# Kernel tuning notes

Measured on AMD Instinct MI355X. Metric: run time of the kernel, lower is better.

## Reference

```python
import jax, jax.numpy as jnp
import numpy as np

BASE_R = 0.1      # base_radius (compared against squared distances)
K = 20            # PositionEncoder k
H = 0.1           # dilated_ball_query bandwidth
EPS_BN = 1e-5


def _gelu(x):
    return jax.nn.gelu(x, approximate=False)  # torch nn.GELU default (erf)


def _bn(x, g, b):
    # eval-mode BatchNorm (running_mean=0, running_var=1), channel axis = 1
    shape = (1, -1) + (1,) * (x.ndim - 2)
    scale = g / np.float32(np.sqrt(1.0 + EPS_BN))
    return x * scale.reshape(shape) + b.reshape(shape)


def _conv1x1(x, w):
    # pointwise conv (no bias): w [out_c, in_c], x [B, in_c, ...]
    return jnp.einsum('oc,bc...->bo...', w, x)


def _l1norm(x, axis):
    # F.normalize(p=1): divide by L1 norm clamped to 1e-12
    return x / jnp.maximum(jnp.sum(jnp.abs(x), axis=axis, keepdims=True), 1e-12)


def _forward(xyz, w_q, g_q, b_q, w_k, g_k, b_k, w_v, g_v, b_v,
             w_pe, b_pe, g_pe, bb_pe, w_m1, g_m1, b_m1, w_m2, g_m2, b_m2,
             w_out, g_out, b_out):
    B, _, N = xyz.shape
    # ---- pairwise squared distances [B,N,N] ----
    sq = jnp.sum(xyz * xyz, axis=1)
    dist = -2.0 * jnp.einsum('bcn,bcm->bnm', xyz, xyz) + sq[:, :, None] + sq[:, None, :]
    # ---- dilated ball query (sigma=1) ----
    gauss = jnp.exp(-dist / (2.0 * H * H))
    kd = jnp.sum(gauss, axis=-1, keepdims=True)                 # [B,N,1]
    kd_score = kd / (jnp.max(kd, axis=1, keepdims=True) + 1e-9)
    radius = BASE_R + BASE_R * kd_score                         # max_radius = 2*base
    keep = dist < radius                                        # [B,N,N]
    # ---- masked attention (emb_cent == emb_x == cat(xyz, xyz)) ----
    emb = jnp.concatenate([xyz, xyz], axis=1)                   # [B,6,N]
    q = _bn(_conv1x1(emb, w_q), g_q, b_q)                       # [B,1,N]
    k_ = _bn(_conv1x1(emb, w_k), g_k, b_k)                      # [B,1,N]
    scores = jnp.einsum('bhn,bhm->bnm', q, k_)                  # [B,N,N]
    scores = jnp.where(keep, scores, -1e9)
    adj = jax.nn.softmax(scores, axis=-1)
    adj = _l1norm(_l1norm(adj, 1), -1)                          # doubly L1-normalized
    # ---- graph smoothing + value conv ----
    smoothed = jnp.einsum('bcn,bnm->bcm', xyz, adj)
    variation = smoothed - xyz
    v = _bn(_conv1x1(jnp.concatenate([variation, xyz], axis=1), w_v), g_v, b_v)  # [B,64,N]
    # ---- position encoder: ball-query top-k neighbor gather ----
    ar = jnp.arange(N, dtype=jnp.int32)[None, None, :]
    idx = jnp.where(dist > radius, N, ar)                       # mark out-of-ball with N
    idx = jnp.sort(idx, axis=-1)[:, :, :K]                      # k nearest-index in-ball
    idx = jnp.where(idx == N, idx[:, :, :1], idx)               # pad with first neighbor
    grouped = jax.vmap(lambda f, i: f[:, i])(xyz, idx)          # [B,3,N,K]
    pts = jnp.broadcast_to(xyz[:, :, :, None], grouped.shape)
    pf = jnp.concatenate([pts, grouped, grouped - pts], axis=1)  # [B,9,N,K]
    pf = _conv1x1(pf, w_pe) + b_pe[None, :, None, None]          # conv2d 1x1 with bias
    pf = _gelu(_bn(pf, g_pe, bb_pe))
    pf = jnp.max(pf, axis=-1)                                    # [B,out/8,N]
    pf = _gelu(_bn(_conv1x1(pf, w_m1), g_m1, b_m1))              # [B,out/4,N]
    pos = _bn(_conv1x1(pf, w_m2), g_m2, b_m2)                    # [B,out,N]
    out = _gelu(v + pos)
    return _bn(_conv1x1(out, w_out), g_out, b_out)               # [B,32,N]


def setup_inputs() -> dict:
    key = jax.random.key(0)
    ks = iter(jax.random.split(key, 40))
    B, N, OC = 4, 4096, 64

    def w(shape):
        return jax.random.normal(next(ks), shape, jnp.float32) / np.float32(np.sqrt(shape[-1]))

    def gb(c):
        g = 1.0 + 0.1 * jax.random.normal(next(ks), (c,), jnp.float32)
        b = 0.1 * jax.random.normal(next(ks), (c,), jnp.float32)
        return g, b

    xyz = jax.random.uniform(next(ks), (B, 3, N), jnp.float32)
    g_q, b_q = gb(1)
    g_k, b_k = gb(1)
    g_v, b_v = gb(OC)
    g_pe, bb_pe = gb(OC // 8)
    g_m1, b_m1 = gb(OC // 4)
    g_m2, b_m2 = gb(OC)
    g_out, b_out = gb(32)
    return {
        'xyz': xyz,
        'w_q': w((1, 6)), 'g_q': g_q, 'b_q': b_q,
        'w_k': w((1, 6)), 'g_k': g_k, 'b_k': b_k,
        'w_v': w((OC, 6)), 'g_v': g_v, 'b_v': b_v,
        'w_pe': w((OC // 8, 9)), 'b_pe': 0.1 * jax.random.normal(next(ks), (OC // 8,), jnp.float32),
        'g_pe': g_pe, 'bb_pe': bb_pe,
        'w_m1': w((OC // 4, OC // 8)), 'g_m1': g_m1, 'b_m1': b_m1,
        'w_m2': w((OC, OC // 4)), 'g_m2': g_m2, 'b_m2': b_m2,
        'w_out': w((32, OC)), 'g_out': g_out, 'b_out': b_out,
    }


def reference(xyz, w_q, g_q, b_q, w_k, g_k, b_k, w_v, g_v, b_v,
              w_pe, b_pe, g_pe, bb_pe, w_m1, g_m1, b_m1, w_m2, g_m2, b_m2,
              w_out, g_out, b_out):
    return _forward(xyz, w_q, g_q, b_q, w_k, g_k, b_k, w_v, g_v, b_v,
                    w_pe, b_pe, g_pe, bb_pe, w_m1, g_m1, b_m1, w_m2, g_m2, b_m2,
                    w_out, g_out, b_out)
```

## Files before the change

### kernel.cpp

```cpp
#include <hip/hip_runtime.h>
#include <math.h>

#define BB 4
#define NN 4096
#define KNBR 20
#define BN (BB * NN)
#define NSLICE 8
#define SLEN (NN / NSLICE)
#define JPW (SLEN / 16)

__device__ __forceinline__ float gelu_f(float x) {
    return 0.5f * x * (1.0f + erff(x * 0.70710678118654752440f));
}

__global__ void k0_prep(const float* __restrict__ xyz,
                        const float* __restrict__ w_q, const float* __restrict__ g_q, const float* __restrict__ b_q,
                        const float* __restrict__ w_k, const float* __restrict__ g_k, const float* __restrict__ b_k,
                        float* __restrict__ qv, float* __restrict__ kv, float4* __restrict__ pts4) {
    int t = blockIdx.x * blockDim.x + threadIdx.x;
    if (t >= BN) return;
    int b = t / NN, n = t % NN;
    const float* base = xyz + (size_t)b * 3 * NN;
    float x = base[n], y = base[NN + n], z = base[2 * NN + n];
    float sq = x * x + y * y + z * z;
    const float invs = rsqrtf(1.0f + 1e-5f);
    float qr = x * (w_q[0] + w_q[3]) + y * (w_q[1] + w_q[4]) + z * (w_q[2] + w_q[5]);
    float kr = x * (w_k[0] + w_k[3]) + y * (w_k[1] + w_k[4]) + z * (w_k[2] + w_k[5]);
    qv[t] = qr * (g_q[0] * invs) + b_q[0];
    kv[t] = kr * (g_k[0] * invs) + b_k[0];
    pts4[t] = make_float4(x, y, z, sq);
}


__global__ __launch_bounds__(1024, 8)
void p1_kd(const float4* __restrict__ pts4, float* __restrict__ part) {
    __shared__ float s_red[16][256];
    int tid = threadIdx.x;
    int wave = __builtin_amdgcn_readfirstlane(tid >> 6);
    int lane = tid & 63;
    int g = blockIdx.x >> 3, slice = blockIdx.x & 7;
    int b = g >> 4;
    const float4* rb = pts4 + (size_t)b * NN + slice * SLEN + wave * JPW;
    float4 fr[4];
    float acc[4] = {0.f, 0.f, 0.f, 0.f};
    #pragma unroll
    for (int rr = 0; rr < 4; ++rr) fr[rr] = pts4[g * 256 + rr * 64 + lane];
    #pragma unroll 4
    for (int j = 0; j < JPW; ++j) {
        float4 fc = rb[j];
        #pragma unroll
        for (int rr = 0; rr < 4; ++rr) {
            float dot = fr[rr].x * fc.x + fr[rr].y * fc.y + fr[rr].z * fc.z;
            float d = fmaf(-2.0f, dot, fr[rr].w) + fc.w;
            acc[rr] += __expf(-50.0f * d);
        }
    }
    #pragma unroll
    for (int rr = 0; rr < 4; ++rr) s_red[wave][rr * 64 + lane] = acc[rr];
    __syncthreads();
    if (tid < 256) {
        float s = 0.f;
        #pragma unroll
        for (int w = 0; w < 16; ++w) s += s_red[w][tid];
        part[slice * BN + g * 256 + tid] = s;
    }
}

__global__ void k2_radius(const float* __restrict__ part, const float4* __restrict__ pts4,
                          const float* __restrict__ qv, const float* __restrict__ kv,
                          float* __restrict__ radius, float4* __restrict__ recB) {
    int b = blockIdx.x;
    int t = threadIdx.x;
    float kdv[4];
    float mx = -1e30f;
    #pragma unroll
    for (int j = 0; j < 4; ++j) {
        int n = b * NN + j * 1024 + t;
        float s = 0.f;
        #pragma unroll
        for (int c = 0; c < NSLICE; ++c) s += part[c * BN + n];
        kdv[j] = s;
        mx = fmaxf(mx, s);
    }
    __shared__ float red[1024];
    red[t] = mx;
    __syncthreads();
    for (int s = 512; s > 0; s >>= 1) {
        if (t < s) red[t] = fmaxf(red[t], red[t + s]);
        __syncthreads();
    }
    float kmax = red[0];
    #pragma unroll
    for (int j = 0; j < 4; ++j) {
        int n = b * NN + j * 1024 + t;
        float rad = 0.1f + 0.1f * (kdv[j] / (kmax + 1e-9f));
        radius[n] = rad;
        recB[2 * n] = pts4[n];
        recB[2 * n + 1] = make_float4(kv[n], qv[n], rad, 0.f);
    }
}

__global__ __launch_bounds__(1024, 8)
void p3_Zk7(const float4* __restrict__ recB, const float4* __restrict__ pts4,
            const float* __restrict__ radius, float* __restrict__ part,
            int* __restrict__ idxg) {
    __shared__ float s_red[16][256];
    int tid = threadIdx.x;
    int wave = __builtin_amdgcn_readfirstlane(tid >> 6);
    int lane = tid & 63;
    int g = blockIdx.x >> 3, slice = blockIdx.x & 7;
    int b = g >> 4;
    const float4* rb = recB + ((size_t)b * NN + slice * SLEN + wave * JPW) * 2;
    float4 fr[4];
    float q[4], rad[4];
    float acc[4] = {0.f, 0.f, 0.f, 0.f};
    #pragma unroll
    for (int rr = 0; rr < 4; ++rr) {
        int r = g * 256 + rr * 64 + lane;
        fr[rr] = recB[2 * r];
        float4 a = recB[2 * r + 1];
        q[rr] = a.y;
        rad[rr] = a.z;
    }
    #pragma unroll 4
    for (int j = 0; j < JPW; ++j) {
        float4 fc = rb[2 * j];
        float4 an = rb[2 * j + 1];
        #pragma unroll
        for (int rr = 0; rr < 4; ++rr) {
            float dot = fr[rr].x * fc.x + fr[rr].y * fc.y + fr[rr].z * fc.z;
            float d = fmaf(-2.0f, dot, fr[rr].w) + fc.w;
            float e = __expf(q[rr] * an.x);
            acc[rr] += (d < rad[rr]) ? e : 0.f;
        }
    }
    #pragma unroll
    for (int rr = 0; rr < 4; ++rr) s_red[wave][rr * 64 + lane] = acc[rr];
    __syncthreads();
    if (tid < 256) {
        float s = 0.f;
        #pragma unroll
        for (int w = 0; w < 16; ++w) s += s_red[w][tid];
        part[slice * BN + g * 256 + tid] = s;
    }
    int gw = blockIdx.x * 16 + wave;
    for (int rr = 0; rr < 2; ++rr) {
        int row7 = gw * 2 + rr;
        int b7 = row7 / NN;
        const float4* p7 = pts4 + (size_t)b7 * NN;
        float4 f7 = pts4[row7];
        float rad7 = radius[row7];
        int total = 0, firstm = 0;
        bool have = false;
        unsigned long long lmask = (1ULL << lane) - 1ULL;
        for (int i = 0; i < NN / 64 && total < KNBR; ++i) {
            int m = i * 64 + lane;
            float4 fc = p7[m];
            float dot = f7.x * fc.x + f7.y * fc.y + f7.z * fc.z;
            float d = fmaf(-2.0f, dot, f7.w) + fc.w;
            bool inb = !(d > rad7);
            unsigned long long mask = __ballot(inb);
            if (!have && mask != 0ULL) {
                int src7 = __ffsll(mask) - 1;
                firstm = __shfl(m, src7);
                have = true;
            }
            int pos = total + (int)__popcll(mask & lmask);
            if (inb && pos < KNBR) idxg[(size_t)row7 * KNBR + pos] = m;
            total += (int)__popcll(mask);
        }
        if (total < KNBR && lane >= total && lane < KNBR)
            idxg[(size_t)row7 * KNBR + lane] = firstm;
    }
}

__global__ void r3_Z(const float* __restrict__ part, const float4* __restrict__ pts4,
                     const float* __restrict__ qv, const float* __restrict__ radius,
                     float* __restrict__ Z, float4* __restrict__ recC) {
    int t = blockIdx.x * blockDim.x + threadIdx.x;
    float s = 0.f;
    #pragma unroll
    for (int c = 0; c < NSLICE; ++c) s += part[c * BN + t];
    Z[t] = s;
    recC[2 * t] = pts4[t];
    recC[2 * t + 1] = make_float4(qv[t], radius[t], __logf(s), 0.f);
}

__global__ __launch_bounds__(1024, 8)
void p4_colsum(const float4* __restrict__ recC, const float4* __restrict__ recB,
               float* __restrict__ part) {
    __shared__ float s_red[16][256];
    int tid = threadIdx.x;
    int wave = __builtin_amdgcn_readfirstlane(tid >> 6);
    int lane = tid & 63;
    int g = blockIdx.x >> 3, slice = blockIdx.x & 7;
    int b = g >> 4;
    const float4* rb = recC + ((size_t)b * NN + slice * SLEN + wave * JPW) * 2;
    float4 fcc[4];
    float km[4];
    float acc[4] = {0.f, 0.f, 0.f, 0.f};
    #pragma unroll
    for (int rr = 0; rr < 4; ++rr) {
        int c = g * 256 + rr * 64 + lane;
        fcc[rr] = recB[2 * c];
        km[rr] = recB[2 * c + 1].x;
    }
    #pragma unroll 4
    for (int j = 0; j < JPW; ++j) {
        float4 fc = rb[2 * j];
        float4 an = rb[2 * j + 1];
        #pragma unroll
        for (int rr = 0; rr < 4; ++rr) {
            float dot = fc.x * fcc[rr].x + fc.y * fcc[rr].y + fc.z * fcc[rr].z;
            float d = fmaf(-2.0f, dot, fc.w) + fcc[rr].w;
            float e = __expf(an.x * km[rr] - an.z);
            acc[rr] += (d < an.y) ? e : 0.f;
        }
    }
    #pragma unroll
    for (int rr = 0; rr < 4; ++rr) s_red[wave][rr * 64 + lane] = acc[rr];
    __syncthreads();
    if (tid < 256) {
        float s = 0.f;
        #pragma unroll
        for (int w = 0; w < 16; ++w) s += s_red[w][tid];
        part[slice * BN + g * 256 + tid] = s;
    }
}

__global__ void r4_colsum(const float* __restrict__ part, const float4* __restrict__ pts4,
                          const float* __restrict__ kv, float* __restrict__ colsum,
                          float4* __restrict__ recD) {
    int t = blockIdx.x * blockDim.x + threadIdx.x;
    float s = 0.f;
    #pragma unroll
    for (int c = 0; c < NSLICE; ++c) s += part[c * BN + t];
    s = fmaxf(s, 1e-12f);
    colsum[t] = s;
    recD[2 * t] = pts4[t];
    recD[2 * t + 1] = make_float4(kv[t], __logf(s), 0.f, 0.f);
}

__global__ __launch_bounds__(1024, 8)
void p5_rs(const float4* __restrict__ recD, const float4* __restrict__ recB,
           float* __restrict__ part) {
    __shared__ float s_red[16][256];
    int tid = threadIdx.x;
    int wave = __builtin_amdgcn_readfirstlane(tid >> 6);
    int lane = tid & 63;
    int g = blockIdx.x >> 3, slice = blockIdx.x & 7;
    int b = g >> 4;
    const float4* rb = recD + ((size_t)b * NN + slice * SLEN + wave * JPW) * 2;
    float4 fr[4];
    float q[4], rad[4];
    float acc[4] = {0.f, 0.f, 0.f, 0.f};
    #pragma unroll
    for (int rr = 0; rr < 4; ++rr) {
        int r = g * 256 + rr * 64 + lane;
        fr[rr] = recB[2 * r];
        float4 a = recB[2 * r + 1];
        q[rr] = a.y;
        rad[rr] = a.z;
    }
    #pragma unroll 4
    for (int j = 0; j < JPW; ++j) {
        float4 fc = rb[2 * j];
        float4 an = rb[2 * j + 1];
        #pragma unroll
        for (int rr = 0; rr < 4; ++rr) {
            float dot = fr[rr].x * fc.x + fr[rr].y * fc.y + fr[rr].z * fc.z;
            float d = fmaf(-2.0f, dot, fr[rr].w) + fc.w;
            float e = __expf(q[rr] * an.x - an.y);
            acc[rr] += (d < rad[rr]) ? e : 0.f;
        }
    }
    #pragma unroll
    for (int rr = 0; rr < 4; ++rr) s_red[wave][rr * 64 + lane] = acc[rr];
    __syncthreads();
    if (tid < 256) {
        float s = 0.f;
        #pragma unroll
        for (int w = 0; w < 16; ++w) s += s_red[w][tid];
        part[slice * BN + g * 256 + tid] = s;
    }
}

__global__ void r5_rs(const float* __restrict__ part, const float* __restrict__ Z,
                      const float4* __restrict__ recC, const float4* __restrict__ pts4,
                      float4* __restrict__ recE) {
    int t = blockIdx.x * blockDim.x + threadIdx.x;
    float s = 0.f;
    #pragma unroll
    for (int c = 0; c < NSLICE; ++c) s += part[c * BN + t];
    float rs = fmaxf(s / Z[t], 1e-12f);
    float4 a = recC[2 * t + 1];
    recE[2 * t] = pts4[t];
    recE[2 * t + 1] = make_float4(a.x, a.y, a.z + __logf(rs), 0.f);
}

__global__ __launch_bounds__(1024, 8)
void p6_smooth(const float4* __restrict__ recE, const float4* __restrict__ recB,
               float* __restrict__ partx, float* __restrict__ party,
               float* __restrict__ partz) {
    __shared__ float s_rx[16][256];
    __shared__ float s_ry[16][256];
    __shared__ float s_rz[16][256];
    int tid = threadIdx.x;
    int wave = __builtin_amdgcn_readfirstlane(tid >> 6);
    int lane = tid & 63;
    int g = blockIdx.x >> 3, slice = blockIdx.x & 7;
    int b = g >> 4;
    const float4* rb = recE + ((size_t)b * NN + slice * SLEN + wave * JPW) * 2;
    float4 fcc[4];
    float km[4];
    float ax[4] = {0.f, 0.f, 0.f, 0.f};
    float ay[4] = {0.f, 0.f, 0.f, 0.f};
    float az[4] = {0.f, 0.f, 0.f, 0.f};
    #pragma unroll
    for (int rr = 0; rr < 4; ++rr) {
        int c = g * 256 + rr * 64 + lane;
        fcc[rr] = recB[2 * c];
        km[rr] = recB[2 * c + 1].x;
    }
    #pragma unroll 2
    for (int j = 0; j < JPW; ++j) {
        float4 fc = rb[2 * j];
        float4 an = rb[2 * j + 1];
        #pragma unroll
        for (int rr = 0; rr < 4; ++rr) {
            float dot = fc.x * fcc[rr].x + fc.y * fcc[rr].y + fc.z * fcc[rr].z;
            float d = fmaf(-2.0f, dot, fc.w) + fcc[rr].w;
            float w = __expf(an.x * km[rr] - an.z);
            w = (d < an.y) ? w : 0.f;
            ax[rr] += fc.x * w;
            ay[rr] += fc.y * w;
            az[rr] += fc.z * w;
        }
    }
    #pragma unroll
    for (int rr = 0; rr < 4; ++rr) {
        s_rx[wave][rr * 64 + lane] = ax[rr];
        s_ry[wave][rr * 64 + lane] = ay[rr];
        s_rz[wave][rr * 64 + lane] = az[rr];
    }
    __syncthreads();
    if (tid < 256) {
        float sx = 0.f, sy = 0.f, sz = 0.f;
        #pragma unroll
        for (int w = 0; w < 16; ++w) {
            sx += s_rx[w][tid];
            sy += s_ry[w][tid];
            sz += s_rz[w][tid];
        }
        int o = slice * BN + g * 256 + tid;
        partx[o] = sx;
        party[o] = sy;
        partz[o] = sz;
    }
}

__global__ void k8_final(const float* __restrict__ xyz,
                         const float* __restrict__ partx, const float* __restrict__ party,
                         const float* __restrict__ partz, const float* __restrict__ colsum,
                         const int* __restrict__ idxg,
                         const float* __restrict__ w_v, const float* __restrict__ g_v, const float* __restrict__ b_v,
                         const float* __restrict__ w_pe, const float* __restrict__ b_pe,
                         const float* __restrict__ g_pe, const float* __restrict__ bb_pe,
                         const float* __restrict__ w_m1, const float* __restrict__ g_m1, const float* __restrict__ b_m1,
                         const float* __restrict__ w_m2, const float* __restrict__ g_m2, const float* __restrict__ b_m2,
                         const float* __restrict__ w_out, const float* __restrict__ g_out, const float* __restrict__ b_out,
                         float* __restrict__ out) {
    __shared__ float s_pf8[32][9];
    __shared__ float s_pf16[32][17];
    __shared__ float s_g64[32][65];
    int tid = threadIdx.x;
    int ptL = tid >> 3, o = tid & 7;
    int p = blockIdx.x * 32 + ptL;
    int b = p / NN, n = p % NN;
    const float* xb = xyz + (size_t)b * 3 * NN;
    float x = xb[n], y = xb[NN + n], z = xb[2 * NN + n];
    const float invs = rsqrtf(1.0f + 1e-5f);

    float w0 = w_pe[o * 9 + 0], w1 = w_pe[o * 9 + 1], w2 = w_pe[o * 9 + 2];
    float w3 = w_pe[o * 9 + 3], w4 = w_pe[o * 9 + 4], w5 = w_pe[o * 9 + 5];
    float w6 = w_pe[o * 9 + 6], w7 = w_pe[o * 9 + 7], w8 = w_pe[o * 9 + 8];
    float bp = b_pe[o], gp = g_pe[o] * invs, bbp = bb_pe[o];
    float mx = -1e30f;
    for (int kk = 0; kk < KNBR; ++kk) {
        int j = idxg[(size_t)p * KNBR + kk];
        float gx = xb[j], gy = xb[NN + j], gz = xb[2 * NN + j];
        float dx = gx - x, dy = gy - y, dz = gz - z;
        float s = w0 * x + w1 * y + w2 * z + w3 * gx + w4 * gy + w5 * gz
                + w6 * dx + w7 * dy + w8 * dz + bp;
        s = gelu_f(s * gp + bbp);
        mx = fmaxf(mx, s);
    }
    s_pf8[ptL][o] = mx;
    __syncthreads();

    #pragma unroll
    for (int rr = 0; rr < 2; ++rr) {
        int r = o + rr * 8;
        const float* w = w_m1 + r * 8;
        float s = 0.f;
        #pragma unroll
        for (int c = 0; c < 8; ++c) s += w[c] * s_pf8[ptL][c];
        s_pf16[ptL][r] = gelu_f(s * (g_m1[r] * invs) + b_m1[r]);
    }
    __syncthreads();

    float inv = 1.0f / colsum[p];
    float sx = 0.f, sy = 0.f, sz = 0.f;
    #pragma unroll
    for (int c = 0; c < NSLICE; ++c) {
        sx += partx[c * BN + p];
        sy += party[c * BN + p];
        sz += partz[c * BN + p];
    }
    float vx = sx * inv - x, vy = sy * inv - y, vz = sz * inv - z;
    #pragma unroll
    for (int i = 0; i < 8; ++i) {
        int ch = o * 8 + i;
        const float* wm = w_m2 + ch * 16;
        float pos = 0.f;
        #pragma unroll
        for (int c = 0; c < 16; ++c) pos += wm[c] * s_pf16[ptL][c];
        pos = pos * (g_m2[ch] * invs) + b_m2[ch];
        const float* wv = w_v + ch * 6;
        float vv = wv[0] * vx + wv[1] * vy + wv[2] * vz + wv[3] * x + wv[4] * y + wv[5] * z;
        vv = vv * (g_v[ch] * invs) + b_v[ch];
        s_g64[ptL][ch] = gelu_f(vv + pos);
    }
    __syncthreads();

    #pragma unroll
    for (int i = 0; i < 4; ++i) {
        int ch = o * 4 + i;
        const float* w = w_out + ch * 64;
        float s = 0.f;
        #pragma unroll
        for (int c = 0; c < 64; ++c) s += w[c] * s_g64[ptL][c];
        out[((size_t)b * 32 + ch) * NN + n] = s * (g_out[ch] * invs) + b_out[ch];
    }
}

extern "C" void kernel_launch(void* const* d_in, const int* in_sizes, int n_in,
                              void* d_out, int out_size, void* d_ws, size_t ws_size,
                              hipStream_t stream) {
    const float* xyz  = (const float*)d_in[0];
    const float* w_q  = (const float*)d_in[1];
    const float* g_q  = (const float*)d_in[2];
    const float* b_q  = (const float*)d_in[3];
    const float* w_k  = (const float*)d_in[4];
    const float* g_k  = (const float*)d_in[5];
    const float* b_k  = (const float*)d_in[6];
    const float* w_v  = (const float*)d_in[7];
    const float* g_v  = (const float*)d_in[8];
    const float* b_v  = (const float*)d_in[9];
    const float* w_pe = (const float*)d_in[10];
    const float* b_pe = (const float*)d_in[11];
    const float* g_pe = (const float*)d_in[12];
    const float* bb_pe= (const float*)d_in[13];
    const float* w_m1 = (const float*)d_in[14];
    const float* g_m1 = (const float*)d_in[15];
    const float* b_m1 = (const float*)d_in[16];
    const float* w_m2 = (const float*)d_in[17];
    const float* g_m2 = (const float*)d_in[18];
    const float* b_m2 = (const float*)d_in[19];
    const float* w_out= (const float*)d_in[20];
    const float* g_out= (const float*)d_in[21];
    const float* b_out= (const float*)d_in[22];

    float* ws = (float*)d_ws;
    float*  qv     = ws;
    float*  kv     = ws + (size_t)1  * BN;
    float4* pts4   = (float4*)(ws + (size_t)2  * BN);
    float*  radius = ws + (size_t)6  * BN;
    float*  Zv     = ws + (size_t)7  * BN;
    float*  colsum = ws + (size_t)8  * BN;
    float4* recB   = (float4*)(ws + (size_t)9  * BN);
    float4* recC   = (float4*)(ws + (size_t)17 * BN);
    float4* recD   = (float4*)(ws + (size_t)25 * BN);
    float4* recE   = (float4*)(ws + (size_t)33 * BN);
    int*    idxg   = (int*)   (ws + (size_t)41 * BN);
    float*  part1  = ws + (size_t)61 * BN;
    float*  part3  = ws + (size_t)69 * BN;
    float*  part5  = ws + (size_t)77 * BN;
    float*  part7  = ws + (size_t)85 * BN;
    float*  partx  = ws + (size_t)93 * BN;
    float*  party  = ws + (size_t)101 * BN;
    float*  partz  = ws + (size_t)109 * BN;

    const int PB = (BN / 256) * NSLICE;

    k0_prep<<<BN / 256, 256, 0, stream>>>(xyz, w_q, g_q, b_q, w_k, g_k, b_k, qv, kv, pts4);
    p1_kd<<<PB, 1024, 0, stream>>>(pts4, part1);
    k2_radius<<<BB, 1024, 0, stream>>>(part1, pts4, qv, kv, radius, recB);
    p3_Zk7<<<PB, 1024, 0, stream>>>(recB, pts4, radius, part3, idxg);
    r3_Z<<<BN / 256, 256, 0, stream>>>(part3, pts4, qv, radius, Zv, recC);
    p4_colsum<<<PB, 1024, 0, stream>>>(recC, recB, part5);
    r4_colsum<<<BN / 256, 256, 0, stream>>>(part5, pts4, kv, colsum, recD);
    p5_rs<<<PB, 1024, 0, stream>>>(recD, recB, part7);
    r5_rs<<<BN / 256, 256, 0, stream>>>(part7, Zv, recC, pts4, recE);
    p6_smooth<<<PB, 1024, 0, stream>>>(recE, recB, partx, party, partz);
    k8_final<<<BN / 32, 256, 0, stream>>>(xyz, partx, party, partz, colsum, idxg,
                                          w_v, g_v, b_v,
                                          w_pe, b_pe, g_pe, bb_pe,
                                          w_m1, g_m1, b_m1,
                                          w_m2, g_m2, b_m2,
                                          w_out, g_out, b_out,
                                          (float*)d_out);
}
```

Before: 251.6 us.

## Fold prep and reduction kernels into pass kernels, reuse single record buffer

Removes k0_prep and the three small reduction kernels (r3_Z, r4_colsum, r5_rs). Each pass kernel now sums the previous pass's slice partials for its own column slice into shared memory, and p1 builds point records directly from xyz. The separate per-pass record buffers go away, so every pass reads the one recB buffer. This cuts four kernel launches and several global round trips, at the cost of redundant partial-sum and log work repeated across row-group blocks and strided record reads inside p1.

```diff
diff --git a/kernel.cpp b/kernel.cpp
--- a/kernel.cpp
+++ b/kernel.cpp
@@ -13,41 +13,31 @@
     return 0.5f * x * (1.0f + erff(x * 0.70710678118654752440f));
 }
 
-__global__ void k0_prep(const float* __restrict__ xyz,
-                        const float* __restrict__ w_q, const float* __restrict__ g_q, const float* __restrict__ b_q,
-                        const float* __restrict__ w_k, const float* __restrict__ g_k, const float* __restrict__ b_k,
-                        float* __restrict__ qv, float* __restrict__ kv, float4* __restrict__ pts4) {
-    int t = blockIdx.x * blockDim.x + threadIdx.x;
-    if (t >= BN) return;
-    int b = t / NN, n = t % NN;
-    const float* base = xyz + (size_t)b * 3 * NN;
-    float x = base[n], y = base[NN + n], z = base[2 * NN + n];
-    float sq = x * x + y * y + z * z;
-    const float invs = rsqrtf(1.0f + 1e-5f);
-    float qr = x * (w_q[0] + w_q[3]) + y * (w_q[1] + w_q[4]) + z * (w_q[2] + w_q[5]);
-    float kr = x * (w_k[0] + w_k[3]) + y * (w_k[1] + w_k[4]) + z * (w_k[2] + w_k[5]);
-    qv[t] = qr * (g_q[0] * invs) + b_q[0];
-    kv[t] = kr * (g_k[0] * invs) + b_k[0];
-    pts4[t] = make_float4(x, y, z, sq);
+__device__ __forceinline__ float4 mkrec(const float* __restrict__ xb, int n) {
+    float x = xb[n], y = xb[NN + n], z = xb[2 * NN + n];
+    float sq = fmaf(x, x, fmaf(y, y, z * z));
+    return make_float4(x, y, z, sq);
 }
 
 
 __global__ __launch_bounds__(1024, 8)
-void p1_kd(const float4* __restrict__ pts4, float* __restrict__ part) {
+void p1_kd(const float* __restrict__ xyz, float* __restrict__ part) {
     __shared__ float s_red[16][256];
     int tid = threadIdx.x;
     int wave = __builtin_amdgcn_readfirstlane(tid >> 6);
     int lane = tid & 63;
     int g = blockIdx.x >> 3, slice = blockIdx.x & 7;
     int b = g >> 4;
-    const float4* rb = pts4 + (size_t)b * NN + slice * SLEN + wave * JPW;
+    const float* xb = xyz + (size_t)b * 3 * NN;
+    int nbase = (g & 15) * 256;
     float4 fr[4];
     float acc[4] = {0.f, 0.f, 0.f, 0.f};
     #pragma unroll
-    for (int rr = 0; rr < 4; ++rr) fr[rr] = pts4[g * 256 + rr * 64 + lane];
+    for (int rr = 0; rr < 4; ++rr) fr[rr] = mkrec(xb, nbase + rr * 64 + lane);
+    int m0 = slice * SLEN + wave * JPW;
     #pragma unroll 4
     for (int j = 0; j < JPW; ++j) {
-        float4 fc = rb[j];
+        float4 fc = mkrec(xb, m0 + j);
         #pragma unroll
         for (int rr = 0; rr < 4; ++rr) {
             float dot = fr[rr].x * fc.x + fr[rr].y * fc.y + fr[rr].z * fc.z;
@@ -66,11 +56,14 @@
     }
 }
 
-__global__ void k2_radius(const float* __restrict__ part, const float4* __restrict__ pts4,
-                          const float* __restrict__ qv, const float* __restrict__ kv,
-                          float* __restrict__ radius, float4* __restrict__ recB) {
+__global__ void k2_radius(const float* __restrict__ part, const float* __restrict__ xyz,
+                          const float* __restrict__ w_q, const float* __restrict__ g_q, const float* __restrict__ b_q,
+                          const float* __restrict__ w_k, const float* __restrict__ g_k, const float* __restrict__ b_k,
+                          float4* __restrict__ recB) {
     int b = blockIdx.x;
     int t = threadIdx.x;
+    const float* xb = xyz + (size_t)b * 3 * NN;
+    const float invs = rsqrtf(1.0f + 1e-5f);
     float kdv[4];
     float mx = -1e30f;
     #pragma unroll
@@ -92,17 +85,21 @@
     float kmax = red[0];
     #pragma unroll
     for (int j = 0; j < 4; ++j) {
-        int n = b * NN + j * 1024 + t;
+        int nl = j * 1024 + t;
+        int n = b * NN + nl;
         float rad = 0.1f + 0.1f * (kdv[j] / (kmax + 1e-9f));
-        radius[n] = rad;
-        recB[2 * n] = pts4[n];
-        recB[2 * n + 1] = make_float4(kv[n], qv[n], rad, 0.f);
+        float4 r = mkrec(xb, nl);
+        float qr = r.x * (w_q[0] + w_q[3]) + r.y * (w_q[1] + w_q[4]) + r.z * (w_q[2] + w_q[5]);
+        float kr = r.x * (w_k[0] + w_k[3]) + r.y * (w_k[1] + w_k[4]) + r.z * (w_k[2] + w_k[5]);
+        float q = qr * (g_q[0] * invs) + b_q[0];
+        float k = kr * (g_k[0] * invs) + b_k[0];
+        recB[2 * n] = r;
+        recB[2 * n + 1] = make_float4(k, q, rad, 0.f);
     }
 }
 
 __global__ __launch_bounds__(1024, 8)
-void p3_Zk7(const float4* __restrict__ recB, const float4* __restrict__ pts4,
-            const float* __restrict__ radius, float* __restrict__ part,
+void p3_Zk7(const float4* __restrict__ recB, float* __restrict__ part,
             int* __restrict__ idxg) {
     __shared__ float s_red[16][256];
     int tid = threadIdx.x;
@@ -147,15 +144,15 @@
     for (int rr = 0; rr < 2; ++rr) {
         int row7 = gw * 2 + rr;
         int b7 = row7 / NN;
-        const float4* p7 = pts4 + (size_t)b7 * NN;
-        float4 f7 = pts4[row7];
-        float rad7 = radius[row7];
+        const float4* p7 = recB + (size_t)b7 * NN * 2;
+        float4 f7 = recB[2 * row7];
+        float rad7 = recB[2 * row7 + 1].z;
         int total = 0, firstm = 0;
         bool have = false;
         unsigned long long lmask = (1ULL << lane) - 1ULL;
         for (int i = 0; i < NN / 64 && total < KNBR; ++i) {
             int m = i * 64 + lane;
-            float4 fc = p7[m];
+            float4 fc = p7[2 * m];
             float dot = f7.x * fc.x + f7.y * fc.y + f7.z * fc.z;
             float d = fmaf(-2.0f, dot, f7.w) + fc.w;
             bool inb = !(d > rad7);
@@ -174,28 +171,24 @@
     }
 }
 
-__global__ void r3_Z(const float* __restrict__ part, const float4* __restrict__ pts4,
-                     const float* __restrict__ qv, const float* __restrict__ radius,
-                     float* __restrict__ Z, float4* __restrict__ recC) {
-    int t = blockIdx.x * blockDim.x + threadIdx.x;
-    float s = 0.f;
-    #pragma unroll
-    for (int c = 0; c < NSLICE; ++c) s += part[c * BN + t];
-    Z[t] = s;
-    recC[2 * t] = pts4[t];
-    recC[2 * t + 1] = make_float4(qv[t], radius[t], __logf(s), 0.f);
-}
-
 __global__ __launch_bounds__(1024, 8)
-void p4_colsum(const float4* __restrict__ recC, const float4* __restrict__ recB,
+void p4_colsum(const float4* __restrict__ recB, const float* __restrict__ part3,
                float* __restrict__ part) {
     __shared__ float s_red[16][256];
+    __shared__ float s_lnZ[SLEN];
     int tid = threadIdx.x;
     int wave = __builtin_amdgcn_readfirstlane(tid >> 6);
     int lane = tid & 63;
     int g = blockIdx.x >> 3, slice = blockIdx.x & 7;
     int b = g >> 4;
-    const float4* rb = recC + ((size_t)b * NN + slice * SLEN + wave * JPW) * 2;
+    if (tid < SLEN) {
+        int gn = b * NN + slice * SLEN + tid;
+        float s = 0.f;
+        #pragma unroll
+        for (int c = 0; c < NSLICE; ++c) s += part3[c * BN + gn];
+        s_lnZ[tid] = __logf(s);
+    }
+    const float4* rb = recB + ((size_t)b * NN + slice * SLEN + wave * JPW) * 2;
     float4 fcc[4];
     float km[4];
     float acc[4] = {0.f, 0.f, 0.f, 0.f};
@@ -205,16 +198,18 @@
         fcc[rr] = recB[2 * c];
         km[rr] = recB[2 * c + 1].x;
     }
+    __syncthreads();
     #pragma unroll 4
     for (int j = 0; j < JPW; ++j) {
         float4 fc = rb[2 * j];
         float4 an = rb[2 * j + 1];
+        float lnZ = s_lnZ[wave * JPW + j];
         #pragma unroll
         for (int rr = 0; rr < 4; ++rr) {
             float dot = fc.x * fcc[rr].x + fc.y * fcc[rr].y + fc.z * fcc[rr].z;
             float d = fmaf(-2.0f, dot, fc.w) + fcc[rr].w;
-            float e = __expf(an.x * km[rr] - an.z);
-            acc[rr] += (d < an.y) ? e : 0.f;
+            float e = __expf(an.y * km[rr] - lnZ);
+            acc[rr] += (d < an.z) ? e : 0.f;
         }
     }
     #pragma unroll
@@ -228,29 +223,24 @@
     }
 }
 
-__global__ void r4_colsum(const float* __restrict__ part, const float4* __restrict__ pts4,
-                          const float* __restrict__ kv, float* __restrict__ colsum,
-                          float4* __restrict__ recD) {
-    int t = blockIdx.x * blockDim.x + threadIdx.x;
-    float s = 0.f;
-    #pragma unroll
-    for (int c = 0; c < NSLICE; ++c) s += part[c * BN + t];
-    s = fmaxf(s, 1e-12f);
-    colsum[t] = s;
-    recD[2 * t] = pts4[t];
-    recD[2 * t + 1] = make_float4(kv[t], __logf(s), 0.f, 0.f);
-}
-
 __global__ __launch_bounds__(1024, 8)
-void p5_rs(const float4* __restrict__ recD, const float4* __restrict__ recB,
+void p5_rs(const float4* __restrict__ recB, const float* __restrict__ part5,
            float* __restrict__ part) {
     __shared__ float s_red[16][256];
+    __shared__ float s_lnc[SLEN];
     int tid = threadIdx.x;
     int wave = __builtin_amdgcn_readfirstlane(tid >> 6);
     int lane = tid & 63;
     int g = blockIdx.x >> 3, slice = blockIdx.x & 7;
     int b = g >> 4;
-    const float4* rb = recD + ((size_t)b * NN + slice * SLEN + wave * JPW) * 2;
+    if (tid < SLEN) {
+        int gm = b * NN + slice * SLEN + tid;
+        float s = 0.f;
+        #pragma unroll
+        for (int c = 0; c < NSLICE; ++c) s += part5[c * BN + gm];
+        s_lnc[tid] = __logf(fmaxf(s, 1e-12f));
+    }
+    const float4* rb = recB + ((size_t)b * NN + slice * SLEN + wave * JPW) * 2;
     float4 fr[4];
     float q[4], rad[4];
     float acc[4] = {0.f, 0.f, 0.f, 0.f};
@@ -262,15 +252,17 @@
         q[rr] = a.y;
         rad[rr] = a.z;
     }
+    __syncthreads();
     #pragma unroll 4
     for (int j = 0; j < JPW; ++j) {
         float4 fc = rb[2 * j];
-        float4 an = rb[2 * j + 1];
+        float km = rb[2 * j + 1].x;
+        float lnc = s_lnc[wave * JPW + j];
         #pragma unroll
         for (int rr = 0; rr < 4; ++rr) {
             float dot = fr[rr].x * fc.x + fr[rr].y * fc.y + fr[rr].z * fc.z;
             float d = fmaf(-2.0f, dot, fr[rr].w) + fc.w;
-            float e = __expf(q[rr] * an.x - an.y);
+            float e = __expf(q[rr] * km - lnc);
             acc[rr] += (d < rad[rr]) ? e : 0.f;
         }
     }
@@ -285,32 +277,32 @@
     }
 }
 
-__global__ void r5_rs(const float* __restrict__ part, const float* __restrict__ Z,
-                      const float4* __restrict__ recC, const float4* __restrict__ pts4,
-                      float4* __restrict__ recE) {
-    int t = blockIdx.x * blockDim.x + threadIdx.x;
-    float s = 0.f;
-    #pragma unroll
-    for (int c = 0; c < NSLICE; ++c) s += part[c * BN + t];
-    float rs = fmaxf(s / Z[t], 1e-12f);
-    float4 a = recC[2 * t + 1];
-    recE[2 * t] = pts4[t];
-    recE[2 * t + 1] = make_float4(a.x, a.y, a.z + __logf(rs), 0.f);
-}
-
 __global__ __launch_bounds__(1024, 8)
-void p6_smooth(const float4* __restrict__ recE, const float4* __restrict__ recB,
+void p6_smooth(const float4* __restrict__ recB, const float* __restrict__ part3,
+               const float* __restrict__ part7,
                float* __restrict__ partx, float* __restrict__ party,
                float* __restrict__ partz) {
     __shared__ float s_rx[16][256];
     __shared__ float s_ry[16][256];
     __shared__ float s_rz[16][256];
+    __shared__ float s_w[SLEN];
     int tid = threadIdx.x;
     int wave = __builtin_amdgcn_readfirstlane(tid >> 6);
     int lane = tid & 63;
     int g = blockIdx.x >> 3, slice = blockIdx.x & 7;
     int b = g >> 4;
-    const float4* rb = recE + ((size_t)b * NN + slice * SLEN + wave * JPW) * 2;
+    if (tid < SLEN) {
+        int gn = b * NN + slice * SLEN + tid;
+        float sZ = 0.f, s7 = 0.f;
+        #pragma unroll
+        for (int c = 0; c < NSLICE; ++c) {
+            sZ += part3[c * BN + gn];
+            s7 += part7[c * BN + gn];
+        }
+        float rs = fmaxf(s7 / sZ, 1e-12f);
+        s_w[tid] = __logf(sZ) + __logf(rs);
+    }
+    const float4* rb = recB + ((size_t)b * NN + slice * SLEN + wave * JPW) * 2;
     float4 fcc[4];
     float km[4];
     float ax[4] = {0.f, 0.f, 0.f, 0.f};
@@ -322,16 +314,18 @@
         fcc[rr] = recB[2 * c];
         km[rr] = recB[2 * c + 1].x;
     }
+    __syncthreads();
     #pragma unroll 2
     for (int j = 0; j < JPW; ++j) {
         float4 fc = rb[2 * j];
         float4 an = rb[2 * j + 1];
+        float wexp = s_w[wave * JPW + j];
         #pragma unroll
         for (int rr = 0; rr < 4; ++rr) {
             float dot = fc.x * fcc[rr].x + fc.y * fcc[rr].y + fc.z * fcc[rr].z;
             float d = fmaf(-2.0f, dot, fc.w) + fcc[rr].w;
-            float w = __expf(an.x * km[rr] - an.z);
-            w = (d < an.y) ? w : 0.f;
+            float w = __expf(an.y * km[rr] - wexp);
+            w = (d < an.z) ? w : 0.f;
             ax[rr] += fc.x * w;
             ay[rr] += fc.y * w;
             az[rr] += fc.z * w;
@@ -361,7 +355,7 @@
 
 __global__ void k8_final(const float* __restrict__ xyz,
                          const float* __restrict__ partx, const float* __restrict__ party,
-                         const float* __restrict__ partz, const float* __restrict__ colsum,
+                         const float* __restrict__ partz, const float* __restrict__ part5,
                          const int* __restrict__ idxg,
                          const float* __restrict__ w_v, const float* __restrict__ g_v, const float* __restrict__ b_v,
                          const float* __restrict__ w_pe, const float* __restrict__ b_pe,
@@ -409,14 +403,15 @@
     }
     __syncthreads();
 
-    float inv = 1.0f / colsum[p];
-    float sx = 0.f, sy = 0.f, sz = 0.f;
+    float cs = 0.f, sx = 0.f, sy = 0.f, sz = 0.f;
     #pragma unroll
     for (int c = 0; c < NSLICE; ++c) {
+        cs += part5[c * BN + p];
         sx += partx[c * BN + p];
         sy += party[c * BN + p];
         sz += partz[c * BN + p];
     }
+    float inv = 1.0f / fmaxf(cs, 1e-12f);
     float vx = sx * inv - x, vy = sy * inv - y, vz = sz * inv - z;
     #pragma unroll
     for (int i = 0; i < 8; ++i) {
@@ -472,38 +467,25 @@
     const float* b_out= (const float*)d_in[22];
 
     float* ws = (float*)d_ws;
-    float*  qv     = ws;
-    float*  kv     = ws + (size_t)1  * BN;
-    float4* pts4   = (float4*)(ws + (size_t)2  * BN);
-    float*  radius = ws + (size_t)6  * BN;
-    float*  Zv     = ws + (size_t)7  * BN;
-    float*  colsum = ws + (size_t)8  * BN;
-    float4* recB   = (float4*)(ws + (size_t)9  * BN);
-    float4* recC   = (float4*)(ws + (size_t)17 * BN);
-    float4* recD   = (float4*)(ws + (size_t)25 * BN);
-    float4* recE   = (float4*)(ws + (size_t)33 * BN);
-    int*    idxg   = (int*)   (ws + (size_t)41 * BN);
-    float*  part1  = ws + (size_t)61 * BN;
-    float*  part3  = ws + (size_t)69 * BN;
-    float*  part5  = ws + (size_t)77 * BN;
-    float*  part7  = ws + (size_t)85 * BN;
-    float*  partx  = ws + (size_t)93 * BN;
-    float*  party  = ws + (size_t)101 * BN;
-    float*  partz  = ws + (size_t)109 * BN;
+    float4* recB   = (float4*)ws;
+    int*    idxg   = (int*)   (ws + (size_t)8  * BN);
+    float*  part1  = ws + (size_t)28 * BN;
+    float*  part3  = ws + (size_t)36 * BN;
+    float*  part5  = ws + (size_t)44 * BN;
+    float*  part7  = ws + (size_t)52 * BN;
+    float*  partx  = ws + (size_t)60 * BN;
+    float*  party  = ws + (size_t)68 * BN;
+    float*  partz  = ws + (size_t)76 * BN;
 
     const int PB = (BN / 256) * NSLICE;
 
-    k0_prep<<<BN / 256, 256, 0, stream>>>(xyz, w_q, g_q, b_q, w_k, g_k, b_k, qv, kv, pts4);
-    p1_kd<<<PB, 1024, 0, stream>>>(pts4, part1);
-    k2_radius<<<BB, 1024, 0, stream>>>(part1, pts4, qv, kv, radius, recB);
-    p3_Zk7<<<PB, 1024, 0, stream>>>(recB, pts4, radius, part3, idxg);
-    r3_Z<<<BN / 256, 256, 0, stream>>>(part3, pts4, qv, radius, Zv, recC);
-    p4_colsum<<<PB, 1024, 0, stream>>>(recC, recB, part5);
-    r4_colsum<<<BN / 256, 256, 0, stream>>>(part5, pts4, kv, colsum, recD);
-    p5_rs<<<PB, 1024, 0, stream>>>(recD, recB, part7);
-    r5_rs<<<BN / 256, 256, 0, stream>>>(part7, Zv, recC, pts4, recE);
-    p6_smooth<<<PB, 1024, 0, stream>>>(recE, recB, partx, party, partz);
-    k8_final<<<BN / 32, 256, 0, stream>>>(xyz, partx, party, partz, colsum, idxg,
+    p1_kd<<<PB, 1024, 0, stream>>>(xyz, part1);
+    k2_radius<<<BB, 1024, 0, stream>>>(part1, xyz, w_q, g_q, b_q, w_k, g_k, b_k, recB);
+    p3_Zk7<<<PB, 1024, 0, stream>>>(recB, part3, idxg);
+    p4_colsum<<<PB, 1024, 0, stream>>>(recB, part3, part5);
+    p5_rs<<<PB, 1024, 0, stream>>>(recB, part5, part7);
+    p6_smooth<<<PB, 1024, 0, stream>>>(recB, part3, part7, partx, party, partz);
+    k8_final<<<BN / 32, 256, 0, stream>>>(xyz, partx, party, partz, part5, idxg,
                                           w_v, g_v, b_v,
                                           w_pe, b_pe, g_pe, bb_pe,
                                           w_m1, g_m1, b_m1,
```

Result: faster. 244.7 us (-2.7%).
